# Kernel optimization log

Measured on AMD Instinct MI355X. Metric: run time of the kernel, lower is better.

Reference implementation:

```python
import jax, jax.numpy as jnp
import numpy as np

B = 256
NUM_CAPS = 2            # digit capsules
N_IN = 6 * 6 * 6 * 32   # 6912 input capsules
D_OUT = 16
D_IN = 8
N_ROUTING = 3           # original loops range(3 - 1) = 2 iterations
EPS = 1e-9


def squash(s):
    # squash along last axis: (|s|^2/(1+|s|^2)) * s/|s|
    n2 = jnp.sum(s * s, axis=-1, keepdims=True)
    return (n2 / (1.0 + n2)) * s / jnp.sqrt(n2 + EPS)


def setup_inputs() -> dict:
    key = jax.random.key(0)
    k1, k2 = jax.random.split(key)
    x = jax.random.normal(k1, (B, N_IN, D_IN), dtype=jnp.float32)
    W = jax.random.normal(k2, (NUM_CAPS, N_IN, D_OUT, D_IN), dtype=jnp.float32) * 0.1
    return {"x": x, "W": W}


def reference(x, W):
    # tile x over the 2 digit capsules + per-(capsule, input-capsule) matvec:
    # u_hat[b,j,n,e] = sum_d W[j,n,e,d] * x[b,n,d]   -> [B, 2, N, 16]
    u_hat = jnp.einsum('bnd,jned->bjne', x, W)
    b_logits = jnp.zeros(u_hat.shape[:3], dtype=x.dtype)  # [B, 2, N]
    v = None
    for _ in range(N_ROUTING - 1):
        c = jax.nn.softmax(b_logits, axis=1)               # softmax over the 2 capsules (dim=1 in source)
        s = jnp.einsum('bjn,bjne->bje', c, u_hat)          # [B, 2, 16]
        v = squash(s)
        b_logits = b_logits + jnp.einsum('bje,bjne->bjn', v, u_hat)
    return v
```

## Files before the change

### kernel.cpp

```cpp
#include <hip/hip_runtime.h>

#define B_ 256
#define J_ 2
#define N_ 6912
#define E_ 16
#define D_ 8
#define NBT 12
#define CGX 576
#define TOT4 (J_*NBT*32)
#define XROW 25
#define XTOT4 (64*XROW)

__device__ __forceinline__ float dpp_row_add16(float v){
  v += __int_as_float(__builtin_amdgcn_update_dpp(0, __float_as_int(v), 0xB1,  0xF, 0xF, true));
  v += __int_as_float(__builtin_amdgcn_update_dpp(0, __float_as_int(v), 0x4E,  0xF, 0xF, true));
  v += __int_as_float(__builtin_amdgcn_update_dpp(0, __float_as_int(v), 0x141, 0xF, 0xF, true));
  v += __int_as_float(__builtin_amdgcn_update_dpp(0, __float_as_int(v), 0x140, 0xF, 0xF, true));
  return v;
}

__device__ __forceinline__ void stageWX(const float* __restrict__ W,
                                        const float* __restrict__ x,
                                        int nb0, int by64, int tid,
                                        float4* __restrict__ Wl,
                                        float4* __restrict__ Xl){
  float4 bw[3], bx[6];
  #pragma unroll
  for (int r=0;r<3;++r){
    const int idx = r*256 + tid;
    const int j  = (idx >= NBT*32) ? 1 : 0;
    const int r4 = idx - j*(NBT*32);
    bw[r] = *(const float4*)(W + ((size_t)j*N_ + nb0)*(E_*D_) + (size_t)r4*4);
  }
  #pragma unroll
  for (int r=0;r<6;++r){
    const int g = r*256 + tid;
    const int brow = g/24, c = g - brow*24;
    bx[r] = *(const float4*)(x + ((size_t)(by64 + brow)*N_ + nb0)*D_ + c*4);
  }
  #pragma unroll
  for (int r=0;r<3;++r){
    const int idx = r*256 + tid;
    const int u = idx & 31;
    Wl[(idx & ~31) | (u ^ (u>>3))] = bw[r];
  }
  #pragma unroll
  for (int r=0;r<6;++r){
    const int g = r*256 + tid;
    const int brow = g/24, c = g - brow*24;
    Xl[brow*XROW + c] = bx[r];
  }
}


__global__ __launch_bounds__(256, 4) void kpass1(const float* __restrict__ x,
                                                 const float* __restrict__ W,
                                                 float* __restrict__ partial)
{
  __shared__ float4 smem4[TOT4 + XTOT4];
  float4* Wl = smem4;
  float4* Xl = smem4 + TOT4;
  const int tid  = threadIdx.x;
  const int lane = tid & 63;
  const int wv   = __builtin_amdgcn_readfirstlane(tid >> 6);
  const int e    = lane & 15;
  const int blo  = lane >> 4;
  const int nb0  = blockIdx.x * NBT;
  const int sA = (e*2)   ^ ((e*2)>>3);
  const int sB = (e*2+1) ^ ((e*2+1)>>3);

  stageWX(W, x, nb0, blockIdx.y*64, tid, Wl, Xl);
  __syncthreads();

  const float4* Xr = Xl + (wv*16 + blo)*XROW;
  float acc0[4] = {0,0,0,0}, acc1[4] = {0,0,0,0};
  #pragma unroll 1
  for (int ni=0; ni<NBT; ++ni){
    const float4 wa0 = Wl[ni*32 + sA];
    const float4 wb0 = Wl[ni*32 + sB];
    const float4 wa1 = Wl[(NBT+ni)*32 + sA];
    const float4 wb1 = Wl[(NBT+ni)*32 + sB];
    #pragma unroll
    for (int k=0;k<4;++k){
      const float4 xa = Xr[k*(4*XROW) + ni*2];
      const float4 xb = Xr[k*(4*XROW) + ni*2 + 1];
      float a0 = acc0[k], a1 = acc1[k];
      a0 = fmaf(wa0.x, xa.x, a0); a0 = fmaf(wa0.y, xa.y, a0);
      a0 = fmaf(wa0.z, xa.z, a0); a0 = fmaf(wa0.w, xa.w, a0);
      a0 = fmaf(wb0.x, xb.x, a0); a0 = fmaf(wb0.y, xb.y, a0);
      a0 = fmaf(wb0.z, xb.z, a0); a0 = fmaf(wb0.w, xb.w, a0);
      a1 = fmaf(wa1.x, xa.x, a1); a1 = fmaf(wa1.y, xa.y, a1);
      a1 = fmaf(wa1.z, xa.z, a1); a1 = fmaf(wa1.w, xa.w, a1);
      a1 = fmaf(wb1.x, xb.x, a1); a1 = fmaf(wb1.y, xb.y, a1);
      a1 = fmaf(wb1.z, xb.z, a1); a1 = fmaf(wb1.w, xb.w, a1);
      acc0[k] = a0; acc1[k] = a1;
    }
  }

  float* dst = partial + (size_t)(blockIdx.x*4 + blockIdx.y)*2048
             + (wv*16 + blo)*32 + e;
  #pragma unroll
  for (int k=0;k<4;++k){ dst[k*128] = acc0[k]; dst[k*128+16] = acc1[k]; }
}

__global__ __launch_bounds__(256, 4) void kpass2(const float* __restrict__ x,
                                                 const float* __restrict__ W,
                                                 const float* __restrict__ v1,
                                                 float* __restrict__ partial)
{
  __shared__ float4 smem4[TOT4 + XTOT4];
  float4* Wl = smem4;
  float4* Xl = smem4 + TOT4;
  const int tid  = threadIdx.x;
  const int lane = tid & 63;
  const int wv   = __builtin_amdgcn_readfirstlane(tid >> 6);
  const int e    = lane & 15;
  const int blo  = lane >> 4;
  const int nb0  = blockIdx.x * NBT;
  const int b0   = blockIdx.y*64 + wv*16 + blo;
  const int sA = (e*2)   ^ ((e*2)>>3);
  const int sB = (e*2+1) ^ ((e*2+1)>>3);

  stageWX(W, x, nb0, blockIdx.y*64, tid, Wl, Xl);
  float vj0[4], vj1[4];
  #pragma unroll
  for (int k=0;k<4;++k){
    vj0[k] = v1[(size_t)(b0 + 4*k)*32 + e];
    vj1[k] = v1[(size_t)(b0 + 4*k)*32 + 16 + e];
  }
  __syncthreads();

  const float4* Xr = Xl + (wv*16 + blo)*XROW;
  float acc0[4] = {0,0,0,0}, acc1[4] = {0,0,0,0};
  #pragma unroll 1
  for (int ni=0; ni<NBT; ++ni){
    const float4 wa0 = Wl[ni*32 + sA];
    const float4 wb0 = Wl[ni*32 + sB];
    const float4 wa1 = Wl[(NBT+ni)*32 + sA];
    const float4 wb1 = Wl[(NBT+ni)*32 + sB];
    #pragma unroll
    for (int k=0;k<4;++k){
      const float4 xa = Xr[k*(4*XROW) + ni*2];
      const float4 xb = Xr[k*(4*XROW) + ni*2 + 1];
      float a0, a1;
      a0 = wa0.x*xa.x;          a0 = fmaf(wa0.y, xa.y, a0);
      a0 = fmaf(wa0.z, xa.z, a0); a0 = fmaf(wa0.w, xa.w, a0);
      a0 = fmaf(wb0.x, xb.x, a0); a0 = fmaf(wb0.y, xb.y, a0);
      a0 = fmaf(wb0.z, xb.z, a0); a0 = fmaf(wb0.w, xb.w, a0);
      a1 = wa1.x*xa.x;          a1 = fmaf(wa1.y, xa.y, a1);
      a1 = fmaf(wa1.z, xa.z, a1); a1 = fmaf(wa1.w, xa.w, a1);
      a1 = fmaf(wb1.x, xb.x, a1); a1 = fmaf(wb1.y, xb.y, a1);
      a1 = fmaf(wb1.z, xb.z, a1); a1 = fmaf(wb1.w, xb.w, a1);
      const float d  = dpp_row_add16(fmaf(vj1[k], a1, -(vj0[k]*a0)));
      const float c0 = __builtin_amdgcn_rcpf(1.f + __expf(d));
      acc0[k] = fmaf(c0,       a0, acc0[k]);
      acc1[k] = fmaf(1.f - c0, a1, acc1[k]);
    }
  }

  float* dst = partial + (size_t)(blockIdx.x*4 + blockIdx.y)*2048
             + (wv*16 + blo)*32 + e;
  #pragma unroll
  for (int k=0;k<4;++k){ dst[k*128] = acc0[k]; dst[k*128+16] = acc1[k]; }
}

template<bool HALF>
__global__ __launch_bounds__(256) void kred(const float* __restrict__ partial,
                                            float* __restrict__ dst)
{
  __shared__ float sh[128];
  const int tid  = threadIdx.x;
  const int o    = blockIdx.x*128 + (tid & 127);
  const int half = tid >> 7;
  const int btile = o >> 11, q = o & 2047;
  const float* p = partial + (size_t)btile*2048 + q + (size_t)half*(CGX/2)*8192;
  float s = 0.f;
  #pragma unroll 24
  for (int cx=0; cx<CGX/2; ++cx) s += p[(size_t)cx*8192];
  if (half) sh[tid & 127] = s;
  __syncthreads();
  if (!half){
    s += sh[tid & 127];
    if (HALF) s *= 0.5f;
    float n2 = s*s;
    #pragma unroll
    for (int m=1; m<16; m<<=1) n2 += __shfl_xor(n2, m);
    dst[o] = s * (n2/(1.f+n2)) * rsqrtf(n2 + 1e-9f);
  }
}

#define NT 512
__global__ __launch_bounds__(NT) void kmono(const float* __restrict__ x,
                                            const float* __restrict__ W,
                                            float* __restrict__ out)
{
  const int b    = blockIdx.x;
  const int tid  = threadIdx.x;
  const int wv   = tid >> 6;
  const int lane = tid & 63;
  __shared__ float wred[8*33];
  __shared__ float vsh[32];

  float acc[32];
  #pragma unroll
  for (int i=0;i<32;++i) acc[i]=0.f;
  for (int n = tid; n < N_; n += NT){
    const float4 xa = *(const float4*)(x + ((size_t)b*N_ + n)*D_);
    const float4 xb = *(const float4*)(x + ((size_t)b*N_ + n)*D_ + 4);
    #pragma unroll
    for (int j=0;j<J_;++j){
      const float* wp = W + ((size_t)j*N_ + n)*(E_*D_);
      #pragma unroll
      for (int e=0;e<E_;++e){
        const float4 wa = *(const float4*)(wp + e*8);
        const float4 wb = *(const float4*)(wp + e*8 + 4);
        float a = acc[j*16+e];
        a = fmaf(wa.x,xa.x,a); a = fmaf(wa.y,xa.y,a); a = fmaf(wa.z,xa.z,a); a = fmaf(wa.w,xa.w,a);
        a = fmaf(wb.x,xb.x,a); a = fmaf(wb.y,xb.y,a); a = fmaf(wb.z,xb.z,a); a = fmaf(wb.w,xb.w,a);
        acc[j*16+e] = a;
      }
    }
  }
  #pragma unroll
  for (int i=0;i<32;++i){
    float v = acc[i];
    #pragma unroll
    for (int off=32; off; off>>=1) v += __shfl_xor(v, off);
    acc[i] = v;
  }
  if (lane == 0){
    #pragma unroll
    for (int i=0;i<32;++i) wred[wv*33 + i] = acc[i];
  }
  __syncthreads();
  if (tid < 32){
    float s = 0.f;
    #pragma unroll
    for (int w=0;w<8;++w) s += wred[w*33 + tid];
    wred[tid] = 0.5f * s;
  }
  __syncthreads();
  if (tid < 32){
    const int j = tid >> 4; float n2 = 0.f;
    #pragma unroll
    for (int e=0;e<16;++e){ const float sv = wred[j*16+e]; n2 = fmaf(sv,sv,n2); }
    vsh[tid] = wred[tid] * (n2/(1.f+n2)) * rsqrtf(n2 + 1e-9f);
  }
  __syncthreads();
  float vv[32];
  #pragma unroll
  for (int i=0;i<32;++i) vv[i] = vsh[i];

  #pragma unroll
  for (int i=0;i<32;++i) acc[i]=0.f;
  for (int n = tid; n < N_; n += NT){
    const float4 xa = *(const float4*)(x + ((size_t)b*N_ + n)*D_);
    const float4 xb = *(const float4*)(x + ((size_t)b*N_ + n)*D_ + 4);
    float u[32];
    #pragma unroll
    for (int j=0;j<J_;++j){
      const float* wp = W + ((size_t)j*N_ + n)*(E_*D_);
      #pragma unroll
      for (int e=0;e<E_;++e){
        const float4 wa = *(const float4*)(wp + e*8);
        const float4 wb = *(const float4*)(wp + e*8 + 4);
        float a;
        a = wa.x*xa.x; a = fmaf(wa.y,xa.y,a); a = fmaf(wa.z,xa.z,a); a = fmaf(wa.w,xa.w,a);
        a = fmaf(wb.x,xb.x,a); a = fmaf(wb.y,xb.y,a); a = fmaf(wb.z,xb.z,a); a = fmaf(wb.w,xb.w,a);
        u[j*16+e] = a;
      }
    }
    float l0=0.f, l1=0.f;
    #pragma unroll
    for (int e=0;e<16;++e){ l0 = fmaf(vv[e],u[e],l0); l1 = fmaf(vv[16+e],u[16+e],l1); }
    const float c0 = 1.f/(1.f + __expf(l1 - l0));
    const float c1 = 1.f - c0;
    #pragma unroll
    for (int e=0;e<16;++e){ acc[e] = fmaf(c0,u[e],acc[e]); acc[16+e] = fmaf(c1,u[16+e],acc[16+e]); }
  }
  #pragma unroll
  for (int i=0;i<32;++i){
    float v = acc[i];
    #pragma unroll
    for (int off=32; off; off>>=1) v += __shfl_xor(v, off);
    acc[i] = v;
  }
  __syncthreads();
  if (lane == 0){
    #pragma unroll
    for (int i=0;i<32;++i) wred[wv*33 + i] = acc[i];
  }
  __syncthreads();
  if (tid < 32){
    float s = 0.f;
    #pragma unroll
    for (int w=0;w<8;++w) s += wred[w*33 + tid];
    wred[tid] = s;
  }
  __syncthreads();
  if (tid < 32){
    const int j = tid >> 4; float n2 = 0.f;
    #pragma unroll
    for (int e=0;e<16;++e){ const float sv = wred[j*16+e]; n2 = fmaf(sv,sv,n2); }
    out[(size_t)b*32 + tid] = wred[tid] * (n2/(1.f+n2)) * rsqrtf(n2 + 1e-9f);
  }
}

extern "C" void kernel_launch(void* const* d_in, const int* in_sizes, int n_in,
                              void* d_out, int out_size, void* d_ws, size_t ws_size,
                              hipStream_t stream)
{
  const float* x = (const float*)d_in[0];
  const float* W = (const float*)d_in[1];
  if (n_in >= 2 && in_sizes[0] < in_sizes[1]){
    x = (const float*)d_in[1]; W = (const float*)d_in[0];
  }
  float* out = (float*)d_out;

  const size_t need = (size_t)(8192 + (size_t)CGX*4*2048) * sizeof(float);

  if (ws_size >= need){
    float* wsf     = (float*)d_ws;
    float* v1      = wsf;
    float* partial = wsf + 8192;
    kpass1<<<dim3(CGX,4), 256, 0, stream>>>(x, W, partial);
    kred<true ><<<64, 256, 0, stream>>>(partial, v1);
    kpass2<<<dim3(CGX,4), 256, 0, stream>>>(x, W, v1, partial);
    kred<false><<<64, 256, 0, stream>>>(partial, out);
  } else {
    kmono<<<B_, NT, 0, stream>>>(x, W, out);
  }
}
```

Baseline: 153.0 us.

## Remap threads to 8 lanes per batch with split-N waves and LDS reduction

Each lane now computes two output elements (e and e+8) for both capsules, so a batch row spans 8 lanes instead of 16. Each wave also handles 32 batches, while wave pairs split the input-capsule loop and combine their partial sums through shared memory before storing. This halves the x LDS reads per FMA and shortens the cross-lane agreement reduction to three DPP steps. In exchange it adds two barriers and an LDS reduction, raises register pressure, and lowers kpass2's occupancy hint to 3.

```diff
diff --git a/kernel.cpp b/kernel.cpp
--- a/kernel.cpp
+++ b/kernel.cpp
@@ -11,12 +11,20 @@
 #define XROW 25
 #define XTOT4 (64*XROW)
 
-__device__ __forceinline__ float dpp_row_add16(float v){
+__device__ __forceinline__ float dpp_add8(float v){
   v += __int_as_float(__builtin_amdgcn_update_dpp(0, __float_as_int(v), 0xB1,  0xF, 0xF, true));
   v += __int_as_float(__builtin_amdgcn_update_dpp(0, __float_as_int(v), 0x4E,  0xF, 0xF, true));
   v += __int_as_float(__builtin_amdgcn_update_dpp(0, __float_as_int(v), 0x141, 0xF, 0xF, true));
-  v += __int_as_float(__builtin_amdgcn_update_dpp(0, __float_as_int(v), 0x140, 0xF, 0xF, true));
   return v;
+}
+
+__device__ __forceinline__ float dot8(const float4 wa, const float4 wb,
+                                      const float4 xa, const float4 xb, float a){
+  a = fmaf(wa.x, xa.x, a); a = fmaf(wa.y, xa.y, a);
+  a = fmaf(wa.z, xa.z, a); a = fmaf(wa.w, xa.w, a);
+  a = fmaf(wb.x, xb.x, a); a = fmaf(wb.y, xb.y, a);
+  a = fmaf(wb.z, xb.z, a); a = fmaf(wb.w, xb.w, a);
+  return a;
 }
 
 __device__ __forceinline__ void stageWX(const float* __restrict__ W,
@@ -63,47 +71,67 @@
   const int tid  = threadIdx.x;
   const int lane = tid & 63;
   const int wv   = __builtin_amdgcn_readfirstlane(tid >> 6);
-  const int e    = lane & 15;
-  const int blo  = lane >> 4;
+  const int eh   = lane & 7;
+  const int bs   = lane >> 3;
+  const int h    = wv >> 1;
+  const int p    = wv & 1;
   const int nb0  = blockIdx.x * NBT;
-  const int sA = (e*2)   ^ ((e*2)>>3);
-  const int sB = (e*2+1) ^ ((e*2+1)>>3);
+
+  const int sA0 = (eh*2)       ^ ((eh*2)>>3);
+  const int sB0 = (eh*2+1)     ^ ((eh*2+1)>>3);
+  const int sA1 = ((eh+8)*2)   ^ (((eh+8)*2)>>3);
+  const int sB1 = ((eh+8)*2+1) ^ (((eh+8)*2+1)>>3);
 
   stageWX(W, x, nb0, blockIdx.y*64, tid, Wl, Xl);
   __syncthreads();
 
-  const float4* Xr = Xl + (wv*16 + blo)*XROW;
-  float acc0[4] = {0,0,0,0}, acc1[4] = {0,0,0,0};
+  const float4* Xr = Xl + (h*32 + bs)*XROW;
+  float aJ0E0[4]={0,0,0,0}, aJ0E1[4]={0,0,0,0}, aJ1E0[4]={0,0,0,0}, aJ1E1[4]={0,0,0,0};
   #pragma unroll 1
-  for (int ni=0; ni<NBT; ++ni){
-    const float4 wa0 = Wl[ni*32 + sA];
-    const float4 wb0 = Wl[ni*32 + sB];
-    const float4 wa1 = Wl[(NBT+ni)*32 + sA];
-    const float4 wb1 = Wl[(NBT+ni)*32 + sB];
-    #pragma unroll
-    for (int k=0;k<4;++k){
-      const float4 xa = Xr[k*(4*XROW) + ni*2];
-      const float4 xb = Xr[k*(4*XROW) + ni*2 + 1];
-      float a0 = acc0[k], a1 = acc1[k];
-      a0 = fmaf(wa0.x, xa.x, a0); a0 = fmaf(wa0.y, xa.y, a0);
-      a0 = fmaf(wa0.z, xa.z, a0); a0 = fmaf(wa0.w, xa.w, a0);
-      a0 = fmaf(wb0.x, xb.x, a0); a0 = fmaf(wb0.y, xb.y, a0);
-      a0 = fmaf(wb0.z, xb.z, a0); a0 = fmaf(wb0.w, xb.w, a0);
-      a1 = fmaf(wa1.x, xa.x, a1); a1 = fmaf(wa1.y, xa.y, a1);
-      a1 = fmaf(wa1.z, xa.z, a1); a1 = fmaf(wa1.w, xa.w, a1);
-      a1 = fmaf(wb1.x, xb.x, a1); a1 = fmaf(wb1.y, xb.y, a1);
-      a1 = fmaf(wb1.z, xb.z, a1); a1 = fmaf(wb1.w, xb.w, a1);
-      acc0[k] = a0; acc1[k] = a1;
-    }
-  }
-
-  float* dst = partial + (size_t)(blockIdx.x*4 + blockIdx.y)*2048
-             + (wv*16 + blo)*32 + e;
-  #pragma unroll
-  for (int k=0;k<4;++k){ dst[k*128] = acc0[k]; dst[k*128+16] = acc1[k]; }
-}
-
-__global__ __launch_bounds__(256, 4) void kpass2(const float* __restrict__ x,
+  for (int ni=p; ni<NBT; ni+=2){
+    const float4 w00a = Wl[ni*32 + sA0],       w00b = Wl[ni*32 + sB0];
+    const float4 w01a = Wl[ni*32 + sA1],       w01b = Wl[ni*32 + sB1];
+    const float4 w10a = Wl[(NBT+ni)*32 + sA0], w10b = Wl[(NBT+ni)*32 + sB0];
+    const float4 w11a = Wl[(NBT+ni)*32 + sA1], w11b = Wl[(NBT+ni)*32 + sB1];
+    #pragma unroll
+    for (int k=0;k<4;++k){
+      const float4 xa = Xr[k*(8*XROW) + ni*2];
+      const float4 xb = Xr[k*(8*XROW) + ni*2 + 1];
+      aJ0E0[k] = dot8(w00a,w00b, xa,xb, aJ0E0[k]);
+      aJ0E1[k] = dot8(w01a,w01b, xa,xb, aJ0E1[k]);
+      aJ1E0[k] = dot8(w10a,w10b, xa,xb, aJ1E0[k]);
+      aJ1E1[k] = dot8(w11a,w11b, xa,xb, aJ1E1[k]);
+    }
+  }
+
+  __syncthreads();
+  float* red = (float*)smem4;
+  if (p == 1){
+    #pragma unroll
+    for (int k=0;k<4;++k){
+      const int base = h*1056 + (8*k+bs)*33 + eh;
+      red[base]      = aJ0E0[k];
+      red[base + 8]  = aJ0E1[k];
+      red[base + 16] = aJ1E0[k];
+      red[base + 24] = aJ1E1[k];
+    }
+  }
+  __syncthreads();
+  if (p == 0){
+    float* dst = partial + (size_t)(blockIdx.x*4 + blockIdx.y)*2048;
+    #pragma unroll
+    for (int k=0;k<4;++k){
+      const int base = h*1056 + (8*k+bs)*33 + eh;
+      const int go   = (h*32 + 8*k + bs)*32 + eh;
+      dst[go]      = aJ0E0[k] + red[base];
+      dst[go + 8]  = aJ0E1[k] + red[base + 8];
+      dst[go + 16] = aJ1E0[k] + red[base + 16];
+      dst[go + 24] = aJ1E1[k] + red[base + 24];
+    }
+  }
+}
+
+__global__ __launch_bounds__(256, 3) void kpass2(const float* __restrict__ x,
                                                  const float* __restrict__ W,
                                                  const float* __restrict__ v1,
                                                  float* __restrict__ partial)
@@ -114,54 +142,85 @@
   const int tid  = threadIdx.x;
   const int lane = tid & 63;
   const int wv   = __builtin_amdgcn_readfirstlane(tid >> 6);
-  const int e    = lane & 15;
-  const int blo  = lane >> 4;
+  const int eh   = lane & 7;
+  const int bs   = lane >> 3;
+  const int h    = wv >> 1;
+  const int p    = wv & 1;
   const int nb0  = blockIdx.x * NBT;
-  const int b0   = blockIdx.y*64 + wv*16 + blo;
-  const int sA = (e*2)   ^ ((e*2)>>3);
-  const int sB = (e*2+1) ^ ((e*2+1)>>3);
-
-  stageWX(W, x, nb0, blockIdx.y*64, tid, Wl, Xl);
-  float vj0[4], vj1[4];
+  const int b0g  = blockIdx.y*64;
+
+  const int sA0 = (eh*2)       ^ ((eh*2)>>3);
+  const int sB0 = (eh*2+1)     ^ ((eh*2+1)>>3);
+  const int sA1 = ((eh+8)*2)   ^ (((eh+8)*2)>>3);
+  const int sB1 = ((eh+8)*2+1) ^ (((eh+8)*2+1)>>3);
+
+  stageWX(W, x, nb0, b0g, tid, Wl, Xl);
+  float v00[4], v01[4], v10[4], v11[4];
   #pragma unroll
   for (int k=0;k<4;++k){
-    vj0[k] = v1[(size_t)(b0 + 4*k)*32 + e];
-    vj1[k] = v1[(size_t)(b0 + 4*k)*32 + 16 + e];
-  }
-  __syncthreads();
-
-  const float4* Xr = Xl + (wv*16 + blo)*XROW;
-  float acc0[4] = {0,0,0,0}, acc1[4] = {0,0,0,0};
+    const size_t vb = (size_t)(b0g + h*32 + 8*k + bs)*32 + eh;
+    v00[k] = v1[vb];
+    v01[k] = v1[vb + 8];
+    v10[k] = v1[vb + 16];
+    v11[k] = v1[vb + 24];
+  }
+  __syncthreads();
+
+  const float4* Xr = Xl + (h*32 + bs)*XROW;
+  float aJ0E0[4]={0,0,0,0}, aJ0E1[4]={0,0,0,0}, aJ1E0[4]={0,0,0,0}, aJ1E1[4]={0,0,0,0};
   #pragma unroll 1
-  for (int ni=0; ni<NBT; ++ni){
-    const float4 wa0 = Wl[ni*32 + sA];
-    const float4 wb0 = Wl[ni*32 + sB];
-    const float4 wa1 = Wl[(NBT+ni)*32 + sA];
-    const float4 wb1 = Wl[(NBT+ni)*32 + sB];
-    #pragma unroll
-    for (int k=0;k<4;++k){
-      const float4 xa = Xr[k*(4*XROW) + ni*2];
-      const float4 xb = Xr[k*(4*XROW) + ni*2 + 1];
-      float a0, a1;
-      a0 = wa0.x*xa.x;          a0 = fmaf(wa0.y, xa.y, a0);
-      a0 = fmaf(wa0.z, xa.z, a0); a0 = fmaf(wa0.w, xa.w, a0);
-      a0 = fmaf(wb0.x, xb.x, a0); a0 = fmaf(wb0.y, xb.y, a0);
-      a0 = fmaf(wb0.z, xb.z, a0); a0 = fmaf(wb0.w, xb.w, a0);
-      a1 = wa1.x*xa.x;          a1 = fmaf(wa1.y, xa.y, a1);
-      a1 = fmaf(wa1.z, xa.z, a1); a1 = fmaf(wa1.w, xa.w, a1);
-      a1 = fmaf(wb1.x, xb.x, a1); a1 = fmaf(wb1.y, xb.y, a1);
-      a1 = fmaf(wb1.z, xb.z, a1); a1 = fmaf(wb1.w, xb.w, a1);
-      const float d  = dpp_row_add16(fmaf(vj1[k], a1, -(vj0[k]*a0)));
-      const float c0 = __builtin_amdgcn_rcpf(1.f + __expf(d));
-      acc0[k] = fmaf(c0,       a0, acc0[k]);
-      acc1[k] = fmaf(1.f - c0, a1, acc1[k]);
-    }
-  }
-
-  float* dst = partial + (size_t)(blockIdx.x*4 + blockIdx.y)*2048
-             + (wv*16 + blo)*32 + e;
-  #pragma unroll
-  for (int k=0;k<4;++k){ dst[k*128] = acc0[k]; dst[k*128+16] = acc1[k]; }
+  for (int ni=p; ni<NBT; ni+=2){
+    const float4 w00a = Wl[ni*32 + sA0],       w00b = Wl[ni*32 + sB0];
+    const float4 w01a = Wl[ni*32 + sA1],       w01b = Wl[ni*32 + sB1];
+    const float4 w10a = Wl[(NBT+ni)*32 + sA0], w10b = Wl[(NBT+ni)*32 + sB0];
+    const float4 w11a = Wl[(NBT+ni)*32 + sA1], w11b = Wl[(NBT+ni)*32 + sB1];
+    #pragma unroll
+    for (int k=0;k<4;++k){
+      const float4 xa = Xr[k*(8*XROW) + ni*2];
+      const float4 xb = Xr[k*(8*XROW) + ni*2 + 1];
+      const float u00 = dot8(w00a,w00b, xa,xb, 0.f);
+      const float u01 = dot8(w01a,w01b, xa,xb, 0.f);
+      const float u10 = dot8(w10a,w10b, xa,xb, 0.f);
+      const float u11 = dot8(w11a,w11b, xa,xb, 0.f);
+      float t = v10[k]*u10;
+      t = fmaf(v11[k], u11, t);
+      t = fmaf(-v00[k], u00, t);
+      t = fmaf(-v01[k], u01, t);
+      t = dpp_add8(t);
+      const float c0 = __builtin_amdgcn_rcpf(1.f + __expf(t));
+      const float c1 = 1.f - c0;
+      aJ0E0[k] = fmaf(c0, u00, aJ0E0[k]);
+      aJ0E1[k] = fmaf(c0, u01, aJ0E1[k]);
+      aJ1E0[k] = fmaf(c1, u10, aJ1E0[k]);
+      aJ1E1[k] = fmaf(c1, u11, aJ1E1[k]);
+    }
+  }
+
+  __syncthreads();
+  float* red = (float*)smem4;
+  if (p == 1){
+    #pragma unroll
+    for (int k=0;k<4;++k){
+      const int base = h*1056 + (8*k+bs)*33 + eh;
+      red[base]      = aJ0E0[k];
+      red[base + 8]  = aJ0E1[k];
+      red[base + 16] = aJ1E0[k];
+      red[base + 24] = aJ1E1[k];
+    }
+  }
+  __syncthreads();
+  if (p == 0){
+    float* dst = partial + (size_t)(blockIdx.x*4 + blockIdx.y)*2048;
+    #pragma unroll
+    for (int k=0;k<4;++k){
+      const int base = h*1056 + (8*k+bs)*33 + eh;
+      const int go   = (h*32 + 8*k + bs)*32 + eh;
+      dst[go]      = aJ0E0[k] + red[base];
+      dst[go + 8]  = aJ0E1[k] + red[base + 8];
+      dst[go + 16] = aJ1E0[k] + red[base + 16];
+      dst[go + 24] = aJ1E1[k] + red[base + 24];
+    }
+  }
 }
 
 template<bool HALF>
```

After: 144.9 us (median of 2 runs). 5.3% less time.

## Register-tile pass kernels over 8 outputs x 4 batches per lane with DPP x-broadcast

Applied to the files above, without the earlier changes.

Each lane now computes a 32-accumulator register tile (2 capsules x 4 output dims x 4 batch rows) instead of 2x4, and broadcasts x values across quad lanes via DPP quad_perm rather than reloading them from LDS. Waves split the input-capsule loop, and their partial sums are combined through shared memory at the end. The aim is to cut LDS read traffic per FMA and shorten the agreement reduction from a 16-lane to a 4-lane DPP sum. In exchange it needs far more registers (kpass2 launch bounds drop to 2 blocks per SM) and adds a cross-wave LDS reduction plus extra barriers.

```diff
diff --git a/kernel.cpp b/kernel.cpp
--- a/kernel.cpp
+++ b/kernel.cpp
@@ -11,12 +11,31 @@
 #define XROW 25
 #define XTOT4 (64*XROW)
 
-__device__ __forceinline__ float dpp_row_add16(float v){
-  v += __int_as_float(__builtin_amdgcn_update_dpp(0, __float_as_int(v), 0xB1,  0xF, 0xF, true));
-  v += __int_as_float(__builtin_amdgcn_update_dpp(0, __float_as_int(v), 0x4E,  0xF, 0xF, true));
-  v += __int_as_float(__builtin_amdgcn_update_dpp(0, __float_as_int(v), 0x141, 0xF, 0xF, true));
-  v += __int_as_float(__builtin_amdgcn_update_dpp(0, __float_as_int(v), 0x140, 0xF, 0xF, true));
+__device__ __forceinline__ float dppf(float v, int pat);
+
+template<int PAT>
+__device__ __forceinline__ float4 qb(const float4 v){
+  float4 r;
+  r.x = __int_as_float(__builtin_amdgcn_update_dpp(0, __float_as_int(v.x), PAT, 0xF, 0xF, true));
+  r.y = __int_as_float(__builtin_amdgcn_update_dpp(0, __float_as_int(v.y), PAT, 0xF, 0xF, true));
+  r.z = __int_as_float(__builtin_amdgcn_update_dpp(0, __float_as_int(v.z), PAT, 0xF, 0xF, true));
+  r.w = __int_as_float(__builtin_amdgcn_update_dpp(0, __float_as_int(v.w), PAT, 0xF, 0xF, true));
+  return r;
+}
+
+__device__ __forceinline__ float dpp_add4(float v){
+  v += __int_as_float(__builtin_amdgcn_update_dpp(0, __float_as_int(v), 0xB1, 0xF, 0xF, true));
+  v += __int_as_float(__builtin_amdgcn_update_dpp(0, __float_as_int(v), 0x4E, 0xF, 0xF, true));
   return v;
+}
+
+__device__ __forceinline__ float dot8(const float4 wa, const float4 wb,
+                                      const float4 xa, const float4 xb, float a){
+  a = fmaf(wa.x, xa.x, a); a = fmaf(wa.y, xa.y, a);
+  a = fmaf(wa.z, xa.z, a); a = fmaf(wa.w, xa.w, a);
+  a = fmaf(wb.x, xb.x, a); a = fmaf(wb.y, xb.y, a);
+  a = fmaf(wb.z, xb.z, a); a = fmaf(wb.w, xb.w, a);
+  return a;
 }
 
 __device__ __forceinline__ void stageWX(const float* __restrict__ W,
@@ -63,47 +82,76 @@
   const int tid  = threadIdx.x;
   const int lane = tid & 63;
   const int wv   = __builtin_amdgcn_readfirstlane(tid >> 6);
-  const int e    = lane & 15;
-  const int blo  = lane >> 4;
+  const int eh   = lane & 3;
+  const int bs   = lane >> 2;
   const int nb0  = blockIdx.x * NBT;
-  const int sA = (e*2)   ^ ((e*2)>>3);
-  const int sB = (e*2+1) ^ ((e*2+1)>>3);
+
+  int sA[4], sB[4];
+  #pragma unroll
+  for (int m=0;m<4;++m){
+    const int uA = 2*(eh+4*m), uB = uA+1;
+    sA[m] = uA ^ (uA>>3);
+    sB[m] = uB ^ (uB>>3);
+  }
 
   stageWX(W, x, nb0, blockIdx.y*64, tid, Wl, Xl);
   __syncthreads();
 
-  const float4* Xr = Xl + (wv*16 + blo)*XROW;
-  float acc0[4] = {0,0,0,0}, acc1[4] = {0,0,0,0};
+  const float4* Xr = Xl + (bs + 16*eh)*XROW;
+  float acc[32];
+  #pragma unroll
+  for (int i=0;i<32;++i) acc[i]=0.f;
+
   #pragma unroll 1
-  for (int ni=0; ni<NBT; ++ni){
-    const float4 wa0 = Wl[ni*32 + sA];
-    const float4 wb0 = Wl[ni*32 + sB];
-    const float4 wa1 = Wl[(NBT+ni)*32 + sA];
-    const float4 wb1 = Wl[(NBT+ni)*32 + sB];
-    #pragma unroll
-    for (int k=0;k<4;++k){
-      const float4 xa = Xr[k*(4*XROW) + ni*2];
-      const float4 xb = Xr[k*(4*XROW) + ni*2 + 1];
-      float a0 = acc0[k], a1 = acc1[k];
-      a0 = fmaf(wa0.x, xa.x, a0); a0 = fmaf(wa0.y, xa.y, a0);
-      a0 = fmaf(wa0.z, xa.z, a0); a0 = fmaf(wa0.w, xa.w, a0);
-      a0 = fmaf(wb0.x, xb.x, a0); a0 = fmaf(wb0.y, xb.y, a0);
-      a0 = fmaf(wb0.z, xb.z, a0); a0 = fmaf(wb0.w, xb.w, a0);
-      a1 = fmaf(wa1.x, xa.x, a1); a1 = fmaf(wa1.y, xa.y, a1);
-      a1 = fmaf(wa1.z, xa.z, a1); a1 = fmaf(wa1.w, xa.w, a1);
-      a1 = fmaf(wb1.x, xb.x, a1); a1 = fmaf(wb1.y, xb.y, a1);
-      a1 = fmaf(wb1.z, xb.z, a1); a1 = fmaf(wb1.w, xb.w, a1);
-      acc0[k] = a0; acc1[k] = a1;
-    }
-  }
-
-  float* dst = partial + (size_t)(blockIdx.x*4 + blockIdx.y)*2048
-             + (wv*16 + blo)*32 + e;
-  #pragma unroll
-  for (int k=0;k<4;++k){ dst[k*128] = acc0[k]; dst[k*128+16] = acc1[k]; }
-}
-
-__global__ __launch_bounds__(256, 4) void kpass2(const float* __restrict__ x,
+  for (int t=0; t<3; ++t){
+    const int ni = wv + 4*t;
+    const float4 xoa = Xr[ni*2], xob = Xr[ni*2+1];
+    float4 xa[4], xb[4];
+    xa[0] = qb<0x00>(xoa); xb[0] = qb<0x00>(xob);
+    xa[1] = qb<0x55>(xoa); xb[1] = qb<0x55>(xob);
+    xa[2] = qb<0xAA>(xoa); xb[2] = qb<0xAA>(xob);
+    xa[3] = qb<0xFF>(xoa); xb[3] = qb<0xFF>(xob);
+    #pragma unroll
+    for (int j=0;j<2;++j){
+      #pragma unroll
+      for (int m=0;m<4;++m){
+        const float4 wa = Wl[(j*NBT+ni)*32 + sA[m]];
+        const float4 wb = Wl[(j*NBT+ni)*32 + sB[m]];
+        #pragma unroll
+        for (int k=0;k<4;++k)
+          acc[(j*4+m)*4+k] = dot8(wa,wb, xa[k],xb[k], acc[(j*4+m)*4+k]);
+      }
+    }
+  }
+
+  __syncthreads();
+  float4* mb = smem4;
+  if (wv){
+    #pragma unroll
+    for (int q=0;q<8;++q)
+      mb[(q*3 + (wv-1))*64 + lane] = make_float4(acc[q*4],acc[q*4+1],acc[q*4+2],acc[q*4+3]);
+  }
+  __syncthreads();
+  if (wv == 0){
+    float* dst = partial + (size_t)(blockIdx.x*4 + blockIdx.y)*2048;
+    #pragma unroll
+    for (int q=0;q<8;++q){
+      float4 s = make_float4(acc[q*4],acc[q*4+1],acc[q*4+2],acc[q*4+3]);
+      #pragma unroll
+      for (int w=0;w<3;++w){
+        const float4 o = mb[(q*3+w)*64 + lane];
+        s.x+=o.x; s.y+=o.y; s.z+=o.z; s.w+=o.w;
+      }
+      const int be = (q>>2)*16 + eh + 4*(q&3);
+      dst[(bs     )*32 + be] = s.x;
+      dst[(bs + 16)*32 + be] = s.y;
+      dst[(bs + 32)*32 + be] = s.z;
+      dst[(bs + 48)*32 + be] = s.w;
+    }
+  }
+}
+
+__global__ __launch_bounds__(256, 2) void kpass2(const float* __restrict__ x,
                                                  const float* __restrict__ W,
                                                  const float* __restrict__ v1,
                                                  float* __restrict__ partial)
@@ -114,54 +162,100 @@
   const int tid  = threadIdx.x;
   const int lane = tid & 63;
   const int wv   = __builtin_amdgcn_readfirstlane(tid >> 6);
-  const int e    = lane & 15;
-  const int blo  = lane >> 4;
+  const int eh   = lane & 3;
+  const int bs   = lane >> 2;
   const int nb0  = blockIdx.x * NBT;
-  const int b0   = blockIdx.y*64 + wv*16 + blo;
-  const int sA = (e*2)   ^ ((e*2)>>3);
-  const int sB = (e*2+1) ^ ((e*2+1)>>3);
-
-  stageWX(W, x, nb0, blockIdx.y*64, tid, Wl, Xl);
-  float vj0[4], vj1[4];
-  #pragma unroll
-  for (int k=0;k<4;++k){
-    vj0[k] = v1[(size_t)(b0 + 4*k)*32 + e];
-    vj1[k] = v1[(size_t)(b0 + 4*k)*32 + 16 + e];
-  }
-  __syncthreads();
-
-  const float4* Xr = Xl + (wv*16 + blo)*XROW;
-  float acc0[4] = {0,0,0,0}, acc1[4] = {0,0,0,0};
+  const int b0g  = blockIdx.y*64;
+
+  int sA[4], sB[4];
+  #pragma unroll
+  for (int m=0;m<4;++m){
+    const int uA = 2*(eh+4*m), uB = uA+1;
+    sA[m] = uA ^ (uA>>3);
+    sB[m] = uB ^ (uB>>3);
+  }
+
+  stageWX(W, x, nb0, b0g, tid, Wl, Xl);
+  float vj[32];
+  #pragma unroll
+  for (int j=0;j<2;++j)
+    #pragma unroll
+    for (int m=0;m<4;++m)
+      #pragma unroll
+      for (int k=0;k<4;++k)
+        vj[(j*4+m)*4+k] = v1[(size_t)(b0g + bs + 16*k)*32 + j*16 + eh + 4*m];
+  __syncthreads();
+
+  const float4* Xr = Xl + (bs + 16*eh)*XROW;
+  float acc[32];
+  #pragma unroll
+  for (int i=0;i<32;++i) acc[i]=0.f;
+
   #pragma unroll 1
-  for (int ni=0; ni<NBT; ++ni){
-    const float4 wa0 = Wl[ni*32 + sA];
-    const float4 wb0 = Wl[ni*32 + sB];
-    const float4 wa1 = Wl[(NBT+ni)*32 + sA];
-    const float4 wb1 = Wl[(NBT+ni)*32 + sB];
+  for (int t=0; t<3; ++t){
+    const int ni = wv + 4*t;
+    const float4 xoa = Xr[ni*2], xob = Xr[ni*2+1];
+    float4 xa[4], xb[4];
+    xa[0] = qb<0x00>(xoa); xb[0] = qb<0x00>(xob);
+    xa[1] = qb<0x55>(xoa); xb[1] = qb<0x55>(xob);
+    xa[2] = qb<0xAA>(xoa); xb[2] = qb<0xAA>(xob);
+    xa[3] = qb<0xFF>(xoa); xb[3] = qb<0xFF>(xob);
+    float u[32];
+    #pragma unroll
+    for (int j=0;j<2;++j){
+      #pragma unroll
+      for (int m=0;m<4;++m){
+        const float4 wa = Wl[(j*NBT+ni)*32 + sA[m]];
+        const float4 wb = Wl[(j*NBT+ni)*32 + sB[m]];
+        #pragma unroll
+        for (int k=0;k<4;++k)
+          u[(j*4+m)*4+k] = dot8(wa,wb, xa[k],xb[k], 0.f);
+      }
+    }
     #pragma unroll
     for (int k=0;k<4;++k){
-      const float4 xa = Xr[k*(4*XROW) + ni*2];
-      const float4 xb = Xr[k*(4*XROW) + ni*2 + 1];
-      float a0, a1;
-      a0 = wa0.x*xa.x;          a0 = fmaf(wa0.y, xa.y, a0);
-      a0 = fmaf(wa0.z, xa.z, a0); a0 = fmaf(wa0.w, xa.w, a0);
-      a0 = fmaf(wb0.x, xb.x, a0); a0 = fmaf(wb0.y, xb.y, a0);
-      a0 = fmaf(wb0.z, xb.z, a0); a0 = fmaf(wb0.w, xb.w, a0);
-      a1 = wa1.x*xa.x;          a1 = fmaf(wa1.y, xa.y, a1);
-      a1 = fmaf(wa1.z, xa.z, a1); a1 = fmaf(wa1.w, xa.w, a1);
-      a1 = fmaf(wb1.x, xb.x, a1); a1 = fmaf(wb1.y, xb.y, a1);
-      a1 = fmaf(wb1.z, xb.z, a1); a1 = fmaf(wb1.w, xb.w, a1);
-      const float d  = dpp_row_add16(fmaf(vj1[k], a1, -(vj0[k]*a0)));
-      const float c0 = __builtin_amdgcn_rcpf(1.f + __expf(d));
-      acc0[k] = fmaf(c0,       a0, acc0[k]);
-      acc1[k] = fmaf(1.f - c0, a1, acc1[k]);
-    }
-  }
-
-  float* dst = partial + (size_t)(blockIdx.x*4 + blockIdx.y)*2048
-             + (wv*16 + blo)*32 + e;
-  #pragma unroll
-  for (int k=0;k<4;++k){ dst[k*128] = acc0[k]; dst[k*128+16] = acc1[k]; }
+      float tt = 0.f;
+      #pragma unroll
+      for (int m=0;m<4;++m){
+        tt = fmaf(vj[(4+m)*4+k], u[(4+m)*4+k], tt);
+        tt = fmaf(-vj[m*4+k],    u[m*4+k],     tt);
+      }
+      tt = dpp_add4(tt);
+      const float c0 = __builtin_amdgcn_rcpf(1.f + __expf(tt));
+      const float c1 = 1.f - c0;
+      #pragma unroll
+      for (int m=0;m<4;++m){
+        acc[m*4+k]     = fmaf(c0, u[m*4+k],     acc[m*4+k]);
+        acc[(4+m)*4+k] = fmaf(c1, u[(4+m)*4+k], acc[(4+m)*4+k]);
+      }
+    }
+  }
+
+  __syncthreads();
+  float4* mb = smem4;
+  if (wv){
+    #pragma unroll
+    for (int q=0;q<8;++q)
+      mb[(q*3 + (wv-1))*64 + lane] = make_float4(acc[q*4],acc[q*4+1],acc[q*4+2],acc[q*4+3]);
+  }
+  __syncthreads();
+  if (wv == 0){
+    float* dst = partial + (size_t)(blockIdx.x*4 + blockIdx.y)*2048;
+    #pragma unroll
+    for (int q=0;q<8;++q){
+      float4 s = make_float4(acc[q*4],acc[q*4+1],acc[q*4+2],acc[q*4+3]);
+      #pragma unroll
+      for (int w=0;w<3;++w){
+        const float4 o = mb[(q*3+w)*64 + lane];
+        s.x+=o.x; s.y+=o.y; s.z+=o.z; s.w+=o.w;
+      }
+      const int be = (q>>2)*16 + eh + 4*(q&3);
+      dst[(bs     )*32 + be] = s.x;
+      dst[(bs + 16)*32 + be] = s.y;
+      dst[(bs + 32)*32 + be] = s.z;
+      dst[(bs + 48)*32 + be] = s.w;
+    }
+  }
 }
 
 template<bool HALF>
```

Result: no change. 150.4 us (-1.7%).
